# Performance work log

Measured on AMD Instinct MI355X. Metric: run time of the kernel, lower is better.

The kernel has to match this reference:

```python
import jax, jax.numpy as jnp
import numpy as np

B, L, D = 2, 4096, 1024
H = 8
DK = D // H          # 128 head qk dim (expand_k=1)
DV = 2 * D // H      # 256 head v dim (expand_v=2)
FFN = 4 * D          # 4096
CHUNK = 64
EPS = 1e-6


def _ln(x, w, b):
    mu = x.mean(-1, keepdims=True)
    var = ((x - mu) ** 2).mean(-1, keepdims=True)
    return (x - mu) / jnp.sqrt(var + EPS) * w + b


def _retention(q, k, v):
    # q,k: [B,H,L,DK], v: [B,H,L,DV]; RetNet decayed causal linear attention,
    # computed chunkwise (intra-chunk parallel + inter-chunk recurrent state).
    Bq, Hq, Lq, Dk = q.shape
    Dv = v.shape[-1]
    N = Lq // CHUNK
    b = 1.0 - jnp.exp2(-5.0 - jnp.arange(Hq, dtype=q.dtype))   # [H] per-head decay
    logb = jnp.log(b)
    q = q * (Dk ** -0.5)
    t = jnp.arange(CHUNK, dtype=q.dtype)
    diff = t[:, None] - t[None, :]                              # [C,C]
    mask = jnp.where(diff >= 0, jnp.exp(logb[:, None, None] * diff), 0.0)  # [H,C,C]
    d_q = jnp.exp(logb[:, None] * (t[None, :] + 1.0))           # b^(t+1), [H,C]
    d_k = jnp.exp(logb[:, None] * (CHUNK - 1.0 - t[None, :]))   # b^(C-1-s), [H,C]
    d_c = jnp.exp(logb * CHUNK)                                 # b^C, [H]

    def to_chunks(x):
        return x.reshape(Bq, Hq, N, CHUNK, -1).transpose(2, 0, 1, 3, 4)  # [N,B,H,C,d]

    qc, kc, vc = to_chunks(q), to_chunks(k), to_chunks(v)
    S0 = jnp.zeros((Bq, Hq, Dk, Dv), q.dtype)

    def step(S, inp):
        qi, ki, vi = inp                                        # [B,H,C,*]
        A = jnp.einsum('bhtd,bhsd->bhts', qi, ki) * mask        # intra-chunk scores
        o = jnp.einsum('bhts,bhsv->bhtv', A, vi)
        o = o + jnp.einsum('bhtd,bhdv->bhtv', qi * d_q[None, :, :, None], S)
        S = S * d_c[None, :, None, None] + jnp.einsum('bhsd,bhsv->bhdv', ki * d_k[None, :, :, None], vi)
        return S, o

    _, os = jax.lax.scan(step, S0, (qc, kc, vc))                # os: [N,B,H,C,DV]
    return os.transpose(1, 2, 0, 3, 4).reshape(Bq, Hq, Lq, Dv)


def setup_inputs() -> dict:
    key = jax.random.key(0)
    ks = jax.random.split(key, 8)
    s = 0.02
    return {
        'x': jax.random.normal(ks[0], (B, L, D), jnp.float32),
        'ln1_w': jnp.ones((D,), jnp.float32),
        'ln1_b': jnp.zeros((D,), jnp.float32),
        'Wq': jax.random.normal(ks[1], (D, D), jnp.float32) * s,
        'Wk': jax.random.normal(ks[2], (D, D), jnp.float32) * s,
        'Wv': jax.random.normal(ks[3], (D, 2 * D), jnp.float32) * s,
        'Wo': jax.random.normal(ks[4], (2 * D, D), jnp.float32) * s,
        'ln2_w': jnp.ones((D,), jnp.float32),
        'ln2_b': jnp.zeros((D,), jnp.float32),
        'W1': jax.random.normal(ks[5], (D, FFN), jnp.float32) * s,
        'b1': jnp.zeros((FFN,), jnp.float32),
        'W2': jax.random.normal(ks[6], (FFN, D), jnp.float32) * s,
        'b2': jnp.zeros((D,), jnp.float32),
    }


def reference(x, ln1_w, ln1_b, Wq, Wk, Wv, Wo, ln2_w, ln2_b, W1, b1, W2, b2):
    # retention branch
    h = _ln(x, ln1_w, ln1_b)
    q = (h @ Wq).reshape(B, L, H, DK).transpose(0, 2, 1, 3)
    k = (h @ Wk).reshape(B, L, H, DK).transpose(0, 2, 1, 3)
    v = (h @ Wv).reshape(B, L, H, DV).transpose(0, 2, 1, 3)
    o = _retention(q, k, v)                                      # [B,H,L,DV]
    o = o.transpose(0, 2, 1, 3).reshape(B, L, H * DV)
    x = x + o @ Wo
    # FFN branch (exact gelu, no subln, eval-mode dropout)
    f = _ln(x, ln2_w, ln2_b)
    f = jax.nn.gelu(f @ W1 + b1, approximate=False)
    x = x + (f @ W2 + b2)
    return x
```

## Files before the change

### kernel.cpp

```cpp
#include <hip/hip_runtime.h>
#include <math.h>

typedef short s16;
typedef __attribute__((ext_vector_type(8))) short short8;
typedef __attribute__((ext_vector_type(4))) float f32x4;

__device__ __forceinline__ float bf2f_lo(unsigned u){ return __builtin_bit_cast(float, u << 16); }
__device__ __forceinline__ float bf2f_hi(unsigned u){ return __builtin_bit_cast(float, u & 0xffff0000u); }
__device__ __forceinline__ float bf2f(unsigned short h){ return __builtin_bit_cast(float, (unsigned)h << 16); }
__device__ __forceinline__ s16 f2bf(float f){
  unsigned u = __builtin_bit_cast(unsigned, f);
  u += 0x7fffu + ((u >> 16) & 1u);
  return (s16)(u >> 16);
}
__device__ __forceinline__ void unpack8(int4 v, float* f){
  unsigned a=(unsigned)v.x, b=(unsigned)v.y, c=(unsigned)v.z, d=(unsigned)v.w;
  f[0]=bf2f_lo(a); f[1]=bf2f_hi(a); f[2]=bf2f_lo(b); f[3]=bf2f_hi(b);
  f[4]=bf2f_lo(c); f[5]=bf2f_hi(c); f[6]=bf2f_lo(d); f[7]=bf2f_hi(d);
}
__device__ __forceinline__ void gl2lds16(const s16* g, s16* l){
  __builtin_amdgcn_global_load_lds((const __attribute__((address_space(1))) void*)g,
                                   (__attribute__((address_space(3))) void*)l, 16, 0, 0);
}

__global__ __launch_bounds__(256) void ln_bf16(const float* __restrict__ x,
                                               const float* __restrict__ w,
                                               const float* __restrict__ b,
                                               s16* __restrict__ out){
  int row = blockIdx.x; int t = threadIdx.x;
  const float* xr = x + (size_t)row * 1024;
  float4 v = *(const float4*)(xr + t*4);
  float s = v.x + v.y + v.z + v.w;
  float ss = v.x*v.x + v.y*v.y + v.z*v.z + v.w*v.w;
  for (int o = 32; o > 0; o >>= 1){ s += __shfl_down(s, o, 64); ss += __shfl_down(ss, o, 64); }
  __shared__ float red[8];
  int wid = t >> 6, lane = t & 63;
  if (lane == 0){ red[wid] = s; red[4+wid] = ss; }
  __syncthreads();
  if (t == 0){
    float S = red[0]+red[1]+red[2]+red[3];
    float SS = red[4]+red[5]+red[6]+red[7];
    red[0] = S * (1.f/1024.f);
    red[1] = SS * (1.f/1024.f);
  }
  __syncthreads();
  float mu = red[0];
  float var = red[1] - mu*mu;
  float rstd = rsqrtf(var + 1e-6f);
  float vv[4] = {v.x, v.y, v.z, v.w};
  short4 o4;
  s16 tmp[4];
  #pragma unroll
  for (int i = 0; i < 4; ++i){
    int c = t*4 + i;
    float val = (vv[i] - mu) * rstd * w[c] + b[c];
    tmp[i] = f2bf(val);
  }
  o4.x = tmp[0]; o4.y = tmp[1]; o4.z = tmp[2]; o4.w = tmp[3];
  *(short4*)(out + (size_t)row*1024 + t*4) = o4;
}

__global__ __launch_bounds__(256) void conv_t(const float* __restrict__ W,
                                              s16* __restrict__ Wt,
                                              int K, int N, float scale){
  __shared__ float tile[32][33];
  int n0 = blockIdx.x * 32, k0 = blockIdx.y * 32;
  int tx = threadIdx.x & 31, ty = threadIdx.x >> 5;
  #pragma unroll
  for (int i = 0; i < 4; ++i){
    int r = ty + i*8;
    tile[r][tx] = W[(size_t)(k0 + r)*N + n0 + tx];
  }
  __syncthreads();
  #pragma unroll
  for (int i = 0; i < 4; ++i){
    int r = ty + i*8;
    Wt[(size_t)(n0 + r)*K + k0 + tx] = f2bf(tile[tx][r] * scale);
  }
}

__device__ __forceinline__ void xcd_tile(int tiles_y, int& tx, int& ty){
  int id = blockIdx.x;
  int sy = tiles_y >> 3;
  int xcd = id & 7, p = id >> 3;
  ty = xcd * sy + (p % sy);
  tx = p / sy;
}

#define VMW(n) asm volatile("s_waitcnt vmcnt(" #n ")" ::: "memory")
#define BARR() asm volatile("s_barrier" ::: "memory")

__global__ __launch_bounds__(512,2) void gemm256(const s16* __restrict__ A,
                                                 const s16* __restrict__ Bt,
                                                 int N, int K,
                                                 s16* __restrict__ Cb,
                                                 const float* __restrict__ bias,
                                                 int flags, int tiles_y){
  __shared__ s16 lds[2*4*8192];
  int t = threadIdx.x;
  int tx, ty; xcd_tile(tiles_y, tx, ty);
  int m0 = ty * 256, n0 = tx * 256;
  int w = t >> 6, lane = t & 63;
  int wm = w >> 2, wn = w & 3;
  int lrow = lane & 15, lq = lane >> 4;
  int s = lrow & 7;

  int grow = t >> 3;
  int g = (t & 7) ^ (grow & 7);
  const s16* Ag = A  + (size_t)(m0 + grow) * K + g*8;
  const s16* Bg = Bt + (size_t)(n0 + grow) * K + g*8;
  int wo = w * 512;

  int abase = (wm*64 + lrow) * 64;
  int bbase = (wn*32 + lrow) * 64;
  int sw0 = ((lq ^ s) << 3);
  int sw1 = (((4 + lq) ^ s) << 3);

  f32x4 acc[2][4][2][2];
  #pragma unroll
  for (int a = 0; a < 2; ++a)
    #pragma unroll
    for (int b = 0; b < 4; ++b)
      #pragma unroll
      for (int c = 0; c < 2; ++c)
        #pragma unroll
        for (int d = 0; d < 2; ++d) acc[a][b][c][d] = (f32x4){0.f,0.f,0.f,0.f};

  short8 af[2][4];
  short8 bfr[2][2][2];

#define STG_A(buf,h,kt) do{ \
    gl2lds16(Ag + (size_t)((h)*128    )*K + (kt)*64, lds + ((buf)*4+(h))*8192 + wo); \
    gl2lds16(Ag + (size_t)((h)*128+ 64)*K + (kt)*64, lds + ((buf)*4+(h))*8192 + 4096 + wo); }while(0)
#define STG_B(buf,nh,kt) do{ \
    gl2lds16(Bg + (size_t)((nh)*128    )*K + (kt)*64, lds + ((buf)*4+2+(nh))*8192 + wo); \
    gl2lds16(Bg + (size_t)((nh)*128+ 64)*K + (kt)*64, lds + ((buf)*4+2+(nh))*8192 + 4096 + wo); }while(0)
#define RD_A(buf,mh) do{ const s16* p_ = lds + ((buf)*4+(mh))*8192 + abase; \
    _Pragma("unroll") for (int m_ = 0; m_ < 4; ++m_){ \
      af[0][m_] = *(const short8*)(p_ + m_*1024 + sw0); \
      af[1][m_] = *(const short8*)(p_ + m_*1024 + sw1); } }while(0)
#define RD_B(buf,nh) do{ const s16* p_ = lds + ((buf)*4+2+(nh))*8192 + bbase; \
    _Pragma("unroll") for (int n_ = 0; n_ < 2; ++n_){ \
      bfr[nh][0][n_] = *(const short8*)(p_ + n_*1024 + sw0); \
      bfr[nh][1][n_] = *(const short8*)(p_ + n_*1024 + sw1); } }while(0)
#define MFMA_Q(mh,nh) do{ __builtin_amdgcn_s_setprio(1); \
    _Pragma("unroll") for (int kk_ = 0; kk_ < 2; ++kk_) \
      _Pragma("unroll") for (int m_ = 0; m_ < 4; ++m_) \
        _Pragma("unroll") for (int n_ = 0; n_ < 2; ++n_) \
          acc[mh][m_][nh][n_] = __builtin_amdgcn_mfma_f32_16x16x32_bf16( \
              af[kk_][m_], bfr[nh][kk_][n_], acc[mh][m_][nh][n_], 0, 0, 0); \
    __builtin_amdgcn_s_setprio(0); }while(0)

  int NT = K >> 6;
  STG_A(0,0,0); STG_B(0,0,0); STG_B(0,1,0); STG_A(0,1,0);
  STG_A(1,0,1); STG_B(1,0,1); STG_B(1,1,1);
  VMW(6); BARR();

  for (int kt = 0; kt < NT-2; ++kt){
    int cb = kt & 1, nb = cb ^ 1;
    RD_A(cb,0); RD_B(cb,0);
    STG_A(nb,1,kt+1);
    BARR(); MFMA_Q(0,0); BARR();
    RD_B(cb,1);
    STG_A(cb,0,kt+2);
    BARR(); MFMA_Q(0,1); BARR();
    RD_A(cb,1);
    STG_B(cb,0,kt+2);
    BARR(); MFMA_Q(1,0); BARR();
    STG_B(cb,1,kt+2);
    VMW(6);
    BARR(); MFMA_Q(1,1); BARR();
  }
  {
    int cb = (NT-2) & 1, nb = cb ^ 1;
    RD_A(cb,0); RD_B(cb,0);
    STG_A(nb,1,NT-1);
    BARR(); MFMA_Q(0,0); BARR();
    RD_B(cb,1);
    BARR(); MFMA_Q(0,1); BARR();
    RD_A(cb,1);
    BARR(); MFMA_Q(1,0); BARR();
    VMW(0);
    BARR(); MFMA_Q(1,1); BARR();
  }
  {
    int cb = (NT-1) & 1;
    RD_A(cb,0); RD_B(cb,0);
    BARR(); MFMA_Q(0,0); BARR();
    RD_B(cb,1);
    BARR(); MFMA_Q(0,1); BARR();
    RD_A(cb,1);
    BARR(); MFMA_Q(1,0); BARR();
    MFMA_Q(1,1);
  }
#undef STG_A
#undef STG_B
#undef RD_A
#undef RD_B
#undef MFMA_Q

  bool do_gelu = flags & 1;
  #pragma unroll
  for (int nh = 0; nh < 2; ++nh){
    #pragma unroll
    for (int nj = 0; nj < 2; ++nj){
      int col = n0 + wn*32 + nh*128 + nj*16 + lrow;
      float bcol = bias ? bias[col] : 0.f;
      #pragma unroll
      for (int mh = 0; mh < 2; ++mh){
        #pragma unroll
        for (int m = 0; m < 4; ++m){
          int row_base = m0 + wm*64 + mh*128 + m*16 + lq*4;
          #pragma unroll
          for (int r = 0; r < 4; ++r){
            float val = acc[mh][m][nh][nj][r] + bcol;
            if (do_gelu) val = 0.5f * val * (1.f + erff(val * 0.70710678118654752f));
            Cb[(size_t)(row_base + r) * N + col] = f2bf(val);
          }
        }
      }
    }
  }
}

__global__ __launch_bounds__(512,2) void gemm256h(const s16* __restrict__ A,
                                                  const s16* __restrict__ Bt,
                                                  int N, int K,
                                                  float* __restrict__ Cf,
                                                  s16* __restrict__ Cb,
                                                  const float* __restrict__ bias,
                                                  const float* __restrict__ resid,
                                                  int flags, int tiles_y){
  __shared__ s16 lds[2*3*8192];
  int t = threadIdx.x;
  int tx, ty; xcd_tile(tiles_y, tx, ty);
  int m0 = ty * 256, n0 = tx * 128;
  int w = t >> 6, lane = t & 63;
  int wm = w >> 2, wn = w & 3;
  int lrow = lane & 15, lq = lane >> 4;
  int s = lrow & 7;

  int grow = t >> 3;
  int g = (t & 7) ^ (grow & 7);
  const s16* Ag = A  + (size_t)(m0 + grow) * K + g*8;
  const s16* Bg = Bt + (size_t)(n0 + grow) * K + g*8;
  int wo = w * 512;

  int abase = (wm*64 + lrow) * 64;
  int bbase = (wn*32 + lrow) * 64;
  int sw0 = ((lq ^ s) << 3);
  int sw1 = (((4 + lq) ^ s) << 3);

  f32x4 acc[2][4][2];
  #pragma unroll
  for (int a = 0; a < 2; ++a)
    #pragma unroll
    for (int b = 0; b < 4; ++b)
      #pragma unroll
      for (int c = 0; c < 2; ++c) acc[a][b][c] = (f32x4){0.f,0.f,0.f,0.f};

  short8 af[2][4], bfr[2][2];

#define STG_A(buf,h,kt) do{ \
    gl2lds16(Ag + (size_t)((h)*128    )*K + (kt)*64, lds + ((buf)*3+(h))*8192 + wo); \
    gl2lds16(Ag + (size_t)((h)*128+ 64)*K + (kt)*64, lds + ((buf)*3+(h))*8192 + 4096 + wo); }while(0)
#define STG_B(buf,kt) do{ \
    gl2lds16(Bg + (size_t)0*K  + (kt)*64, lds + ((buf)*3+2)*8192 + wo); \
    gl2lds16(Bg + (size_t)64*K + (kt)*64, lds + ((buf)*3+2)*8192 + 4096 + wo); }while(0)
#define RD_A(buf,mh) do{ const s16* p_ = lds + ((buf)*3+(mh))*8192 + abase; \
    _Pragma("unroll") for (int m_ = 0; m_ < 4; ++m_){ \
      af[0][m_] = *(const short8*)(p_ + m_*1024 + sw0); \
      af[1][m_] = *(const short8*)(p_ + m_*1024 + sw1); } }while(0)
#define RD_B(buf) do{ const s16* p_ = lds + ((buf)*3+2)*8192 + bbase; \
    _Pragma("unroll") for (int n_ = 0; n_ < 2; ++n_){ \
      bfr[0][n_] = *(const short8*)(p_ + n_*1024 + sw0); \
      bfr[1][n_] = *(const short8*)(p_ + n_*1024 + sw1); } }while(0)
#define MFMA_H(mh) do{ __builtin_amdgcn_s_setprio(1); \
    _Pragma("unroll") for (int kk_ = 0; kk_ < 2; ++kk_) \
      _Pragma("unroll") for (int m_ = 0; m_ < 4; ++m_) \
        _Pragma("unroll") for (int n_ = 0; n_ < 2; ++n_) \
          acc[mh][m_][n_] = __builtin_amdgcn_mfma_f32_16x16x32_bf16( \
              af[kk_][m_], bfr[kk_][n_], acc[mh][m_][n_], 0, 0, 0); \
    __builtin_amdgcn_s_setprio(0); }while(0)

  int NT = K >> 6;
  STG_A(0,0,0); STG_B(0,0); STG_A(0,1,0);
  STG_A(1,0,1); STG_B(1,1);
  VMW(4); BARR();

  for (int kt = 0; kt < NT-2; ++kt){
    int cb = kt & 1, nb = cb ^ 1;
    RD_A(cb,0); RD_B(cb);
    STG_A(nb,1,kt+1);
    BARR(); MFMA_H(0); BARR();
    RD_A(cb,1);
    STG_A(cb,0,kt+2); STG_B(cb,kt+2);
    VMW(4);
    BARR(); MFMA_H(1); BARR();
  }
  {
    int cb = (NT-2) & 1, nb = cb ^ 1;
    RD_A(cb,0); RD_B(cb);
    STG_A(nb,1,NT-1);
    BARR(); MFMA_H(0); BARR();
    RD_A(cb,1);
    VMW(0);
    BARR(); MFMA_H(1); BARR();
  }
  {
    int cb = (NT-1) & 1;
    RD_A(cb,0); RD_B(cb);
    BARR(); MFMA_H(0); BARR();
    RD_A(cb,1);
    MFMA_H(1);
  }
#undef STG_A
#undef STG_B
#undef RD_A
#undef RD_B
#undef MFMA_H

  bool do_gelu = flags & 1;
  bool out_bf = flags & 2;
  #pragma unroll
  for (int nj = 0; nj < 2; ++nj){
    int col = n0 + wn*32 + nj*16 + lrow;
    float bcol = bias ? bias[col] : 0.f;
    #pragma unroll
    for (int mh = 0; mh < 2; ++mh){
      #pragma unroll
      for (int m = 0; m < 4; ++m){
        int row_base = m0 + wm*64 + mh*128 + m*16 + lq*4;
        #pragma unroll
        for (int r = 0; r < 4; ++r){
          int grow_ = row_base + r;
          float val = acc[mh][m][nj][r] + bcol;
          if (do_gelu) val = 0.5f * val * (1.f + erff(val * 0.70710678118654752f));
          if (resid) val += resid[(size_t)grow_ * N + col];
          if (out_bf) Cb[(size_t)grow_ * N + col] = f2bf(val);
          else        Cf[(size_t)grow_ * N + col] = val;
        }
      }
    }
  }
}

__global__ __launch_bounds__(256,2) void ret_chunksum(const s16* __restrict__ k,
                                                      const s16* __restrict__ v,
                                                      s16* __restrict__ U){
  int bi = blockIdx.x;
  int h = bi & 7, n = bi >> 3;
  int t = threadIdx.x;
  __shared__ s16 ks[128*72];
  __shared__ s16 vs[256*72];
  float log2b = log2f(1.f - exp2f(-5.f - (float)h));
  const s16* kbase = k + (size_t)(n*64)*4096 + h*128;
  const s16* vbase = v + (size_t)(n*64)*4096 + h*256;
  #pragma unroll
  for (int i = 0; i < 4; ++i){
    int e = i*2048 + t*8;
    int s = e >> 7, dk = e & 127;
    int4 kv = *(const int4*)(kbase + (size_t)s*4096 + dk);
    float f[8]; unpack8(kv, f);
    float dec = exp2f(log2b * (float)(63 - s));
    #pragma unroll
    for (int j = 0; j < 8; ++j) ks[(dk+j)*72 + s] = f2bf(f[j]*dec);
  }
  #pragma unroll
  for (int i = 0; i < 8; ++i){
    int e = i*2048 + t*8;
    int s = e >> 8, dv = e & 255;
    int4 vv = *(const int4*)(vbase + (size_t)s*4096 + dv);
    s16 tmp[8]; *(int4*)tmp = vv;
    #pragma unroll
    for (int j = 0; j < 8; ++j) vs[(dv+j)*72 + s] = tmp[j];
  }
  __syncthreads();
  int w = t >> 6, lane = t & 63;
  int m0w = w*64;
  int lrow = lane & 15, lq = lane >> 4;
  f32x4 acc[4][8];
  #pragma unroll
  for (int mi = 0; mi < 4; ++mi)
    #pragma unroll
    for (int ni = 0; ni < 8; ++ni) acc[mi][ni] = (f32x4){0.f,0.f,0.f,0.f};
  #pragma unroll
  for (int kk = 0; kk < 64; kk += 32){
    short8 af[4], bfr[8];
    #pragma unroll
    for (int mi = 0; mi < 4; ++mi)
      af[mi] = *(short8*)&vs[(m0w + mi*16 + lrow)*72 + kk + lq*8];
    #pragma unroll
    for (int ni = 0; ni < 8; ++ni)
      bfr[ni] = *(short8*)&ks[(ni*16 + lrow)*72 + kk + lq*8];
    #pragma unroll
    for (int mi = 0; mi < 4; ++mi)
      #pragma unroll
      for (int ni = 0; ni < 8; ++ni)
        acc[mi][ni] = __builtin_amdgcn_mfma_f32_16x16x32_bf16(af[mi], bfr[ni], acc[mi][ni], 0, 0, 0);
  }
  s16* Ub = U + ((size_t)(h*64 + n))*32768;
  #pragma unroll
  for (int mi = 0; mi < 4; ++mi)
    #pragma unroll
    for (int ni = 0; ni < 8; ++ni)
      #pragma unroll
      for (int r = 0; r < 4; ++r){
        int row = m0w + mi*16 + lq*4 + r;
        int col = ni*16 + lrow;
        Ub[(size_t)row*128 + col] = f2bf(acc[mi][ni][r]);
      }
}

__global__ __launch_bounds__(256) void ret_scan(s16* __restrict__ US){
  int tid = blockIdx.x*256 + threadIdx.x;
  int h = tid >> 12;
  int rem = tid & 4095;
  int dv = rem >> 4, dk0 = (rem & 15)*8;
  float log2b = log2f(1.f - exp2f(-5.f - (float)h));
  float dc = exp2f(log2b * 64.f);
  s16* base = US + (size_t)h*64*32768 + (size_t)dv*128 + dk0;
  float acc[8] = {0.f,0.f,0.f,0.f,0.f,0.f,0.f,0.f};
  #pragma unroll 4
  for (int n = 0; n < 64; ++n){
    s16* p = base + (size_t)n*32768;
    int4 u4 = *(const int4*)p;
    float uf[8]; unpack8(u4, uf);
    s16 sb[8];
    #pragma unroll
    for (int j = 0; j < 8; ++j) sb[j] = f2bf(acc[j]);
    *(int4*)p = *(int4*)sb;
    #pragma unroll
    for (int j = 0; j < 8; ++j) acc[j] = acc[j]*dc + uf[j];
  }
}

__global__ __launch_bounds__(256,2) void ret_attn(const s16* __restrict__ q,
                                                  const s16* __restrict__ k,
                                                  const s16* __restrict__ v,
                                                  const s16* __restrict__ S,
                                                  s16* __restrict__ o){
  int bi = blockIdx.x;
  int h = bi & 7, n = bi >> 3;
  int t = threadIdx.x;
  int w = t >> 6, lane = t & 63;
  int lrow = lane & 15, lq = lane >> 4;
  float log2b = log2f(1.f - exp2f(-5.f - (float)h));
  __shared__ s16 As[64*72];
  __shared__ s16 vs[256*72];

  const s16* vbase = v + (size_t)(n*64)*4096 + h*256;
  #pragma unroll
  for (int i = 0; i < 8; ++i){
    int e = i*2048 + t*8;
    int s = e >> 8, dv = e & 255;
    int4 vv = *(const int4*)(vbase + (size_t)s*4096 + dv);
    s16 tmp[8]; *(int4*)tmp = vv;
    #pragma unroll
    for (int j = 0; j < 8; ++j) vs[(dv+j)*72 + s] = tmp[j];
  }

  const s16* qbase = q + (size_t)(n*64)*4096 + h*128;
  const s16* kbase = k + (size_t)(n*64)*4096 + h*128;
  short8 qf[4][4];
  #pragma unroll
  for (int ti = 0; ti < 4; ++ti)
    #pragma unroll
    for (int c = 0; c < 4; ++c)
      qf[ti][c] = *(const short8*)(qbase + (size_t)(ti*16 + lrow)*4096 + c*32 + lq*8);
  short8 kf[4];
  #pragma unroll
  for (int c = 0; c < 4; ++c)
    kf[c] = *(const short8*)(kbase + (size_t)(16*w + lrow)*4096 + c*32 + lq*8);
  #pragma unroll
  for (int ti = 0; ti < 4; ++ti){
    f32x4 acc_a = (f32x4){0.f,0.f,0.f,0.f};
    #pragma unroll
    for (int c = 0; c < 4; ++c)
      acc_a = __builtin_amdgcn_mfma_f32_16x16x32_bf16(qf[ti][c], kf[c], acc_a, 0, 0, 0);
    #pragma unroll
    for (int r = 0; r < 4; ++r){
      int ti_idx = ti*16 + lq*4 + r;
      int s_idx = 16*w + lrow;
      int d = ti_idx - s_idx;
      float val = (d >= 0) ? acc_a[r] * exp2f(log2b * (float)d) : 0.f;
      As[ti_idx*72 + s_idx] = f2bf(val);
    }
  }
  __syncthreads();

  f32x4 acc[4][4];
  #pragma unroll
  for (int mi = 0; mi < 4; ++mi)
    #pragma unroll
    for (int nj = 0; nj < 4; ++nj) acc[mi][nj] = (f32x4){0.f,0.f,0.f,0.f};

  const s16* Sbase = S + ((size_t)(h*64 + n)*256 + w*64)*128;
  #pragma unroll
  for (int c = 0; c < 4; ++c){
    short8 bf[4];
    #pragma unroll
    for (int nj = 0; nj < 4; ++nj)
      bf[nj] = *(const short8*)(Sbase + (size_t)(nj*16 + lrow)*128 + c*32 + lq*8);
    #pragma unroll
    for (int mi = 0; mi < 4; ++mi)
      #pragma unroll
      for (int nj = 0; nj < 4; ++nj)
        acc[mi][nj] = __builtin_amdgcn_mfma_f32_16x16x32_bf16(qf[mi][c], bf[nj], acc[mi][nj], 0, 0, 0);
  }
  #pragma unroll
  for (int mi = 0; mi < 4; ++mi){
    #pragma unroll
    for (int r = 0; r < 4; ++r){
      float dq = exp2f(log2b * (float)(mi*16 + lq*4 + r + 1));
      #pragma unroll
      for (int nj = 0; nj < 4; ++nj) acc[mi][nj][r] *= dq;
    }
  }
  #pragma unroll
  for (int c = 0; c < 2; ++c){
    short8 af[4], bf[4];
    #pragma unroll
    for (int mi = 0; mi < 4; ++mi)
      af[mi] = *(short8*)&As[(mi*16 + lrow)*72 + c*32 + lq*8];
    #pragma unroll
    for (int nj = 0; nj < 4; ++nj)
      bf[nj] = *(short8*)&vs[(w*64 + nj*16 + lrow)*72 + c*32 + lq*8];
    #pragma unroll
    for (int mi = 0; mi < 4; ++mi)
      #pragma unroll
      for (int nj = 0; nj < 4; ++nj)
        acc[mi][nj] = __builtin_amdgcn_mfma_f32_16x16x32_bf16(af[mi], bf[nj], acc[mi][nj], 0, 0, 0);
  }
  s16* obase = o + (size_t)(n*64)*2048 + h*256;
  #pragma unroll
  for (int mi = 0; mi < 4; ++mi)
    #pragma unroll
    for (int nj = 0; nj < 4; ++nj)
      #pragma unroll
      for (int r = 0; r < 4; ++r){
        int row = mi*16 + lq*4 + r;
        int col = w*64 + nj*16 + lrow;
        obase[(size_t)row*2048 + col] = f2bf(acc[mi][nj][r]);
      }
}

extern "C" void kernel_launch(void* const* d_in, const int* in_sizes, int n_in,
                              void* d_out, int out_size, void* d_ws, size_t ws_size,
                              hipStream_t stream) {
  (void)in_sizes; (void)n_in; (void)out_size; (void)ws_size;
  const float* x     = (const float*)d_in[0];
  const float* ln1_w = (const float*)d_in[1];
  const float* ln1_b = (const float*)d_in[2];
  const float* Wq    = (const float*)d_in[3];
  const float* Wk    = (const float*)d_in[4];
  const float* Wv    = (const float*)d_in[5];
  const float* Wo    = (const float*)d_in[6];
  const float* ln2_w = (const float*)d_in[7];
  const float* ln2_b = (const float*)d_in[8];
  const float* W1    = (const float*)d_in[9];
  const float* b1    = (const float*)d_in[10];
  const float* W2    = (const float*)d_in[11];
  const float* b2    = (const float*)d_in[12];
  float* out = (float*)d_out;
  char* ws = (char*)d_ws;

  const size_t MB = 1ull << 20;
  s16* Wqkv_t = (s16*)(ws + 0*MB);
  s16* Wo_t = (s16*)(ws + 8*MB);
  s16* W1_t = (s16*)(ws + 12*MB);
  s16* W2_t = (s16*)(ws + 20*MB);
  s16* hbuf = (s16*)(ws + 28*MB);
  s16* h2   = (s16*)(ws + 28*MB);
  s16* qkv  = (s16*)(ws + 44*MB);
  float* x1 = (float*)(ws + 44*MB);
  s16* fb   = (s16*)(ws + 76*MB);
  s16* US   = (s16*)(ws + 108*MB);
  s16* ob   = (s16*)(ws + 140*MB);

  conv_t<<<dim3(32,32),  256, 0, stream>>>(Wq, Wqkv_t, 1024, 1024, 0.08838834764831845f);
  conv_t<<<dim3(32,32),  256, 0, stream>>>(Wk, Wqkv_t + (size_t)1024*1024, 1024, 1024, 1.f);
  conv_t<<<dim3(64,32),  256, 0, stream>>>(Wv, Wqkv_t + (size_t)2048*1024, 1024, 2048, 1.f);
  conv_t<<<dim3(32,64),  256, 0, stream>>>(Wo, Wo_t, 2048, 1024, 1.f);
  conv_t<<<dim3(128,32), 256, 0, stream>>>(W1, W1_t, 1024, 4096, 1.f);
  conv_t<<<dim3(32,128), 256, 0, stream>>>(W2, W2_t, 4096, 1024, 1.f);

  ln_bf16<<<8192, 256, 0, stream>>>(x, ln1_w, ln1_b, hbuf);

  gemm256<<<512, 512, 0, stream>>>(hbuf, Wqkv_t, 4096, 1024, qkv, nullptr, 0, 32);

  for (int b = 0; b < 2; ++b){
    const s16* q_b = qkv + (size_t)b*4096*4096;
    const s16* k_b = q_b + 1024;
    const s16* v_b = q_b + 2048;
    s16* ob_b = ob + (size_t)b*4096*2048;
    ret_chunksum<<<512, 256, 0, stream>>>(k_b, v_b, US);
    ret_scan<<<128, 256, 0, stream>>>(US);
    ret_attn<<<512, 256, 0, stream>>>(q_b, k_b, v_b, US, ob_b);
  }

  gemm256h<<<256, 512, 0, stream>>>(ob, Wo_t, 1024, 2048, x1, nullptr, nullptr, x, 0, 32);
  ln_bf16<<<8192, 256, 0, stream>>>(x1, ln2_w, ln2_b, h2);

  gemm256<<<512, 512, 0, stream>>>(h2, W1_t, 4096, 1024, fb, b1, 1, 32);
  gemm256h<<<256, 512, 0, stream>>>(fb, W2_t, 1024, 4096, out, nullptr, b2, x1, 0, 32);
}
```

Baseline: 604.4 us.

## Double-buffer LDS fragment registers to overlap reads with MFMA in GEMM kernels

Both GEMM kernels now keep two sets of A/B register fragments, so the LDS reads for the next quadrant or half are issued right before the MFMA block on the current fragments. This removes the barrier that previously sat after each MFMA block. The narrow kernel's loop is unrolled by two with fixed buffer indices. The aim is to hide LDS read latency behind matrix math and drop barriers, at the cost of more VGPRs and a possible occupancy loss. It also requires an even tile count in the narrow kernel.

```diff
diff --git a/kernel.cpp b/kernel.cpp
--- a/kernel.cpp
+++ b/kernel.cpp
@@ -126,8 +126,8 @@
         #pragma unroll
         for (int d = 0; d < 2; ++d) acc[a][b][c][d] = (f32x4){0.f,0.f,0.f,0.f};
 
-  short8 af[2][4];
-  short8 bfr[2][2][2];
+  short8 afA[2][4], afB[2][4];
+  short8 bf0[2][2], bf1[2][2];
 
 #define STG_A(buf,h,kt) do{ \
     gl2lds16(Ag + (size_t)((h)*128    )*K + (kt)*64, lds + ((buf)*4+(h))*8192 + wo); \
@@ -135,68 +135,69 @@
 #define STG_B(buf,nh,kt) do{ \
     gl2lds16(Bg + (size_t)((nh)*128    )*K + (kt)*64, lds + ((buf)*4+2+(nh))*8192 + wo); \
     gl2lds16(Bg + (size_t)((nh)*128+ 64)*K + (kt)*64, lds + ((buf)*4+2+(nh))*8192 + 4096 + wo); }while(0)
-#define RD_A(buf,mh) do{ const s16* p_ = lds + ((buf)*4+(mh))*8192 + abase; \
+#define RD_AF(buf,mh,dst) do{ const s16* p_ = lds + ((buf)*4+(mh))*8192 + abase; \
     _Pragma("unroll") for (int m_ = 0; m_ < 4; ++m_){ \
-      af[0][m_] = *(const short8*)(p_ + m_*1024 + sw0); \
-      af[1][m_] = *(const short8*)(p_ + m_*1024 + sw1); } }while(0)
-#define RD_B(buf,nh) do{ const s16* p_ = lds + ((buf)*4+2+(nh))*8192 + bbase; \
+      dst[0][m_] = *(const short8*)(p_ + m_*1024 + sw0); \
+      dst[1][m_] = *(const short8*)(p_ + m_*1024 + sw1); } }while(0)
+#define RD_BF(buf,nh,dst) do{ const s16* p_ = lds + ((buf)*4+2+(nh))*8192 + bbase; \
     _Pragma("unroll") for (int n_ = 0; n_ < 2; ++n_){ \
-      bfr[nh][0][n_] = *(const short8*)(p_ + n_*1024 + sw0); \
-      bfr[nh][1][n_] = *(const short8*)(p_ + n_*1024 + sw1); } }while(0)
-#define MFMA_Q(mh,nh) do{ __builtin_amdgcn_s_setprio(1); \
+      dst[0][n_] = *(const short8*)(p_ + n_*1024 + sw0); \
+      dst[1][n_] = *(const short8*)(p_ + n_*1024 + sw1); } }while(0)
+#define MFMA_Q(mh,nh,A_,B_) do{ __builtin_amdgcn_s_setprio(1); \
     _Pragma("unroll") for (int kk_ = 0; kk_ < 2; ++kk_) \
       _Pragma("unroll") for (int m_ = 0; m_ < 4; ++m_) \
         _Pragma("unroll") for (int n_ = 0; n_ < 2; ++n_) \
           acc[mh][m_][nh][n_] = __builtin_amdgcn_mfma_f32_16x16x32_bf16( \
-              af[kk_][m_], bfr[nh][kk_][n_], acc[mh][m_][nh][n_], 0, 0, 0); \
+              A_[kk_][m_], B_[kk_][n_], acc[mh][m_][nh][n_], 0, 0, 0); \
     __builtin_amdgcn_s_setprio(0); }while(0)
 
   int NT = K >> 6;
   STG_A(0,0,0); STG_B(0,0,0); STG_B(0,1,0); STG_A(0,1,0);
   STG_A(1,0,1); STG_B(1,0,1); STG_B(1,1,1);
   VMW(6); BARR();
+  RD_AF(0,0,afA); RD_BF(0,0,bf0);
 
   for (int kt = 0; kt < NT-2; ++kt){
     int cb = kt & 1, nb = cb ^ 1;
-    RD_A(cb,0); RD_B(cb,0);
     STG_A(nb,1,kt+1);
-    BARR(); MFMA_Q(0,0); BARR();
-    RD_B(cb,1);
+    BARR();
+    RD_BF(cb,1,bf1);
+    MFMA_Q(0,0,afA,bf0);
     STG_A(cb,0,kt+2);
-    BARR(); MFMA_Q(0,1); BARR();
-    RD_A(cb,1);
+    BARR();
+    RD_AF(cb,1,afB);
+    MFMA_Q(0,1,afA,bf1);
     STG_B(cb,0,kt+2);
-    BARR(); MFMA_Q(1,0); BARR();
+    BARR();
+    MFMA_Q(1,0,afB,bf0);
     STG_B(cb,1,kt+2);
     VMW(6);
-    BARR(); MFMA_Q(1,1); BARR();
+    BARR();
+    RD_AF(nb,0,afA); RD_BF(nb,0,bf0);
+    MFMA_Q(1,1,afB,bf1);
   }
   {
     int cb = (NT-2) & 1, nb = cb ^ 1;
-    RD_A(cb,0); RD_B(cb,0);
     STG_A(nb,1,NT-1);
-    BARR(); MFMA_Q(0,0); BARR();
-    RD_B(cb,1);
-    BARR(); MFMA_Q(0,1); BARR();
-    RD_A(cb,1);
-    BARR(); MFMA_Q(1,0); BARR();
+    BARR(); RD_BF(cb,1,bf1); MFMA_Q(0,0,afA,bf0);
+    BARR(); RD_AF(cb,1,afB); MFMA_Q(0,1,afA,bf1);
+    BARR(); MFMA_Q(1,0,afB,bf0);
     VMW(0);
-    BARR(); MFMA_Q(1,1); BARR();
+    BARR();
+    RD_AF(nb,0,afA); RD_BF(nb,0,bf0);
+    MFMA_Q(1,1,afB,bf1);
   }
   {
     int cb = (NT-1) & 1;
-    RD_A(cb,0); RD_B(cb,0);
-    BARR(); MFMA_Q(0,0); BARR();
-    RD_B(cb,1);
-    BARR(); MFMA_Q(0,1); BARR();
-    RD_A(cb,1);
-    BARR(); MFMA_Q(1,0); BARR();
-    MFMA_Q(1,1);
+    BARR(); RD_BF(cb,1,bf1); MFMA_Q(0,0,afA,bf0);
+    BARR(); RD_AF(cb,1,afB); MFMA_Q(0,1,afA,bf1);
+    BARR(); MFMA_Q(1,0,afB,bf0);
+    MFMA_Q(1,1,afB,bf1);
   }
 #undef STG_A
 #undef STG_B
-#undef RD_A
-#undef RD_B
+#undef RD_AF
+#undef RD_BF
 #undef MFMA_Q
 
   bool do_gelu = flags & 1;
@@ -259,7 +260,8 @@
       #pragma unroll
       for (int c = 0; c < 2; ++c) acc[a][b][c] = (f32x4){0.f,0.f,0.f,0.f};
 
-  short8 af[2][4], bfr[2][2];
+  short8 afA[2][4], afB[2][4];
+  short8 bfE[2][2], bfO[2][2];
 
 #define STG_A(buf,h,kt) do{ \
     gl2lds16(Ag + (size_t)((h)*128    )*K + (kt)*64, lds + ((buf)*3+(h))*8192 + wo); \
@@ -267,57 +269,53 @@
 #define STG_B(buf,kt) do{ \
     gl2lds16(Bg + (size_t)0*K  + (kt)*64, lds + ((buf)*3+2)*8192 + wo); \
     gl2lds16(Bg + (size_t)64*K + (kt)*64, lds + ((buf)*3+2)*8192 + 4096 + wo); }while(0)
-#define RD_A(buf,mh) do{ const s16* p_ = lds + ((buf)*3+(mh))*8192 + abase; \
+#define RD_AH(buf,mh,dst) do{ const s16* p_ = lds + ((buf)*3+(mh))*8192 + abase; \
     _Pragma("unroll") for (int m_ = 0; m_ < 4; ++m_){ \
-      af[0][m_] = *(const short8*)(p_ + m_*1024 + sw0); \
-      af[1][m_] = *(const short8*)(p_ + m_*1024 + sw1); } }while(0)
-#define RD_B(buf) do{ const s16* p_ = lds + ((buf)*3+2)*8192 + bbase; \
+      dst[0][m_] = *(const short8*)(p_ + m_*1024 + sw0); \
+      dst[1][m_] = *(const short8*)(p_ + m_*1024 + sw1); } }while(0)
+#define RD_BH(buf,dst) do{ const s16* p_ = lds + ((buf)*3+2)*8192 + bbase; \
     _Pragma("unroll") for (int n_ = 0; n_ < 2; ++n_){ \
-      bfr[0][n_] = *(const short8*)(p_ + n_*1024 + sw0); \
-      bfr[1][n_] = *(const short8*)(p_ + n_*1024 + sw1); } }while(0)
-#define MFMA_H(mh) do{ __builtin_amdgcn_s_setprio(1); \
+      dst[0][n_] = *(const short8*)(p_ + n_*1024 + sw0); \
+      dst[1][n_] = *(const short8*)(p_ + n_*1024 + sw1); } }while(0)
+#define MFMA_H(mh,A_,B_) do{ __builtin_amdgcn_s_setprio(1); \
     _Pragma("unroll") for (int kk_ = 0; kk_ < 2; ++kk_) \
       _Pragma("unroll") for (int m_ = 0; m_ < 4; ++m_) \
         _Pragma("unroll") for (int n_ = 0; n_ < 2; ++n_) \
           acc[mh][m_][n_] = __builtin_amdgcn_mfma_f32_16x16x32_bf16( \
-              af[kk_][m_], bfr[kk_][n_], acc[mh][m_][n_], 0, 0, 0); \
+              A_[kk_][m_], B_[kk_][n_], acc[mh][m_][n_], 0, 0, 0); \
     __builtin_amdgcn_s_setprio(0); }while(0)
 
   int NT = K >> 6;
   STG_A(0,0,0); STG_B(0,0); STG_A(0,1,0);
   STG_A(1,0,1); STG_B(1,1);
   VMW(4); BARR();
-
-  for (int kt = 0; kt < NT-2; ++kt){
-    int cb = kt & 1, nb = cb ^ 1;
-    RD_A(cb,0); RD_B(cb);
-    STG_A(nb,1,kt+1);
-    BARR(); MFMA_H(0); BARR();
-    RD_A(cb,1);
-    STG_A(cb,0,kt+2); STG_B(cb,kt+2);
+  RD_AH(0,0,afA); RD_BH(0,bfE);
+
+  for (int it = 0; it < (NT-2)/2; ++it){
+    int kt = 2*it;
+    STG_A(1,1,kt+1);
+    BARR(); RD_AH(0,1,afB); MFMA_H(0,afA,bfE);
+    STG_A(0,0,kt+2); STG_B(0,kt+2);
     VMW(4);
-    BARR(); MFMA_H(1); BARR();
+    BARR(); RD_AH(1,0,afA); RD_BH(1,bfO); MFMA_H(1,afB,bfE);
+    STG_A(0,1,kt+2);
+    BARR(); RD_AH(1,1,afB); MFMA_H(0,afA,bfO);
+    STG_A(1,0,kt+3); STG_B(1,kt+3);
+    VMW(4);
+    BARR(); RD_AH(0,0,afA); RD_BH(0,bfE); MFMA_H(1,afB,bfO);
   }
   {
-    int cb = (NT-2) & 1, nb = cb ^ 1;
-    RD_A(cb,0); RD_B(cb);
-    STG_A(nb,1,NT-1);
-    BARR(); MFMA_H(0); BARR();
-    RD_A(cb,1);
+    STG_A(1,1,NT-1);
+    BARR(); RD_AH(0,1,afB); MFMA_H(0,afA,bfE);
     VMW(0);
-    BARR(); MFMA_H(1); BARR();
-  }
-  {
-    int cb = (NT-1) & 1;
-    RD_A(cb,0); RD_B(cb);
-    BARR(); MFMA_H(0); BARR();
-    RD_A(cb,1);
-    MFMA_H(1);
+    BARR(); RD_AH(1,0,afA); RD_BH(1,bfO); MFMA_H(1,afB,bfE);
+    BARR(); RD_AH(1,1,afB); MFMA_H(0,afA,bfO);
+    MFMA_H(1,afB,bfO);
   }
 #undef STG_A
 #undef STG_B
-#undef RD_A
-#undef RD_B
+#undef RD_AH
+#undef RD_BH
 #undef MFMA_H
 
   bool do_gelu = flags & 1;
```

Result: no change. 604.2 us (-0.0%).
